# Performance work log

Hardware: AMD Instinct MI355X
Metric: run time of the kernel (lower is better)

Reference implementation:

```python
import jax, jax.numpy as jnp
import numpy as np
import math

B, H, T, D = 4, 16, 577, 1024   # CLIP ViT-L/336: 576 patches + CLS
NEED = 192                      # need_token_num
GROUP = NEED // 4               # 48 PCA components


def setup_inputs():
    key = jax.random.key(0)
    k1, k2 = jax.random.split(key)
    hidden_states = jax.random.normal(k1, (B, T, D), dtype=jnp.float32)
    attn = jax.random.uniform(k2, (B, H, T, T), dtype=jnp.float32)
    attn_weights = attn / attn.sum(-1, keepdims=True)  # row-stochastic attention
    return {"hidden_states": hidden_states, "attn_weights": attn_weights}


def batch_pca(hidden, q):
    # torch.pca_lowrank(sigmoid(h).transpose(2,1)[:,:,1:], q): center columns, top-q right singular vectors
    M = jax.nn.sigmoid(hidden.astype(jnp.float32)).transpose(0, 2, 1)[:, :, 1:]  # [B, D, N]
    Mc = M - M.mean(axis=1, keepdims=True)
    _, _, Vh = jnp.linalg.svd(Mc, full_matrices=False)      # [B, min(D,N), N]
    V = jnp.abs(jnp.transpose(Vh[:, :q, :], (0, 2, 1)))     # [B, N, q]
    belong = jnp.argmax(V, axis=-1)                          # [B, N]
    return V, belong


def batch_similarity_nms(group_sim, scores, threshold):
    # group_sim [B,G,N,N], scores [B,N,G], threshold [B]
    Bn, G, N, _ = group_sim.shape
    bi = jnp.arange(Bn)[:, None]
    gi = jnp.arange(G)[None, :]

    def cond(state):
        return state[0].sum() > 0

    def body(state):
        ns, rs, counts, gs = state
        max_values = ns.max(axis=1)          # [B,G]
        max_idx = jnp.argmax(ns, axis=1)     # [B,G]
        valid = max_values > 0
        sim_row = group_sim[bi, gi, max_idx]  # [B,G,N] row of selected token
        idx_n = jnp.where(valid, max_idx, N)  # sentinel -> dropped
        rs = rs.at[bi, idx_n, gi].set(gs, mode='drop')
        ns = ns.at[bi, idx_n, gi].set(0.0, mode='drop')
        suppress = sim_row > threshold[:, None, None]          # [B,G,N]
        ns = jnp.where(jnp.transpose(suppress, (0, 2, 1)), 0.0, ns)
        return ns, rs, counts + valid.astype(jnp.int32), gs - 1.0

    init = (scores, scores, jnp.zeros((Bn, G), jnp.int32), jnp.float32(1000.0))
    _, rs, counts, _ = jax.lax.while_loop(cond, body, init)
    return counts, rs  # kept-per-group counts, return_scores


def _forward(hs, attn):
    Bn, T_, _ = hs.shape
    N = T_ - 1
    need, G = NEED, GROUP
    hsc = jax.lax.stop_gradient(hs)
    attnc = jax.lax.stop_gradient(attn)

    V, belong = batch_pca(hsc, G)
    cls_sum = attnc[:, :, 0, 1:].sum(axis=1)                  # [B,N] cls attention
    onehot = belong[:, :, None] == jnp.arange(G)[None, None, :]  # [B,N,G]
    scores = jnp.where(onehot, cls_sum[:, :, None], 0.0).astype(jnp.float32)

    x = hsc[:, 1:, :]
    normalized = x / jnp.maximum(jnp.linalg.norm(x, axis=-1, keepdims=True), 1e-12)
    similarity = jnp.einsum('bnd,bmd->bnm', normalized, normalized).astype(jnp.float32)
    triu = jnp.triu(jnp.ones((N, N), bool), k=1)
    sim_mean = (similarity * triu).sum((-1, -2)) / triu.sum()  # [B]

    m = belong[:, None, :] == jnp.arange(G)[None, :, None]     # [B,G,N]
    mask4 = m[:, :, :, None] | m[:, :, None, :]                # row-or-col in group
    group_sim = jnp.where(mask4, similarity[:, None, :, :], 0.0)  # [B,G,N,N]

    keep_counts, ret_scores = batch_similarity_nms(group_sim, scores, (need / 32.0) * sim_mean)

    group_counts = onehot.sum(axis=1).astype(jnp.int32)        # [B,G]
    lower = jnp.minimum(1, group_counts)
    upper = jnp.minimum(jnp.minimum(5 * math.ceil(need / 64), group_counts), keep_counts)

    def ub_cond(u):
        return jnp.any(u.sum(-1) < need)

    def ub_body(u):
        deficient = (u.sum(-1) < need).astype(u.dtype)
        return jnp.minimum(u + deficient[:, None], group_counts)

    upper = jax.lax.while_loop(ub_cond, ub_body, upper)

    other = jnp.maximum(need - lower.sum(-1) - 1, 0)           # [B]
    norm_counts = keep_counts.astype(jnp.float32) / keep_counts.sum(-1, keepdims=True).astype(jnp.float32)
    csum = jnp.cumsum(norm_counts, axis=-1)
    od = jnp.round(csum * other[:, None].astype(jnp.float32)).astype(jnp.int32)
    od = od - jnp.concatenate([jnp.zeros((Bn, 1), jnp.int32), od[:, :-1]], axis=-1)
    token_d0 = jnp.minimum(od + lower, upper)
    sort_idx_g = jnp.argsort(-keep_counts, axis=-1)            # groups by kept count, desc
    target = other + lower.sum(-1)                             # == need-1 per batch
    bi1 = jnp.arange(Bn)

    def f_cond(state):
        return jnp.any(state[0].sum(-1) < target)

    def f_body(state):
        d, fg = state
        deficient = d.sum(-1) < target
        gidx = jnp.take_along_axis(sort_idx_g, jnp.minimum(fg, G - 1)[:, None], axis=1)[:, 0]
        fill = jnp.minimum(upper[bi1, gidx] - d[bi1, gidx], target - d.sum(-1))
        d = d.at[bi1, gidx].add(jnp.where(deficient, fill, 0))
        return d, fg + deficient.astype(fg.dtype)

    token_d, _ = jax.lax.while_loop(f_cond, f_body, (token_d0, jnp.zeros((Bn,), jnp.int32)))

    # top token_d[b,g] indices per group by return_scores, concatenated in group order
    sort_idx = jnp.transpose(jnp.argsort(-ret_scores, axis=1), (0, 2, 1)).astype(jnp.int32)  # [B,G,N]
    take = jnp.arange(N)[None, None, :] < token_d[:, :, None]  # [B,G,N]
    flat_take = take.reshape(Bn, G * N)
    flat_idx = sort_idx.reshape(Bn, G * N)
    L = need - 1  # token_d sums exactly to target == need-1
    pos = jnp.cumsum(flat_take, axis=1) - 1
    pos = jnp.where(flat_take, pos, L)
    gathered = jnp.zeros((Bn, L), jnp.int32).at[bi1[:, None], pos].set(flat_idx, mode='drop')
    batch_indices = jnp.concatenate([jnp.zeros((Bn, 1), jnp.int32), gathered + 1], axis=1)  # [B, need]
    out = jnp.take_along_axis(hs, batch_indices[:, :, None], axis=1)  # [B, need, D]
    return out, batch_indices


def reference(hidden_states, attn_weights):
    return _forward(hidden_states, attn_weights)
```

## Files before the change

kernel.cpp:

```cpp
#include <hip/hip_runtime.h>
#include <math.h>

constexpr int B_ = 4, T_ = 577, N_ = 576, D_ = 1024, G_ = 48, H_ = 16;
constexpr int NEED_ = 192, L_ = 191;
constexpr int TRIU_CNT = N_ * (N_ - 1) / 2;
constexpr int NB_ = 8;
constexpr int NBAR_ = 640;

constexpr size_t OF_MSIG = 0;
constexpr size_t OF_SIM  = OF_MSIG + (size_t)B_*N_*D_*4;
constexpr size_t OF_A    = OF_SIM  + (size_t)B_*N_*N_*4;
constexpr size_t OF_MS   = OF_A    + (size_t)B_*N_*N_*8;
constexpr size_t OF_INVN = OF_MS   + (size_t)B_*N_*8;
constexpr size_t OF_CLS  = OF_INVN + (size_t)B_*N_*8;
constexpr size_t OF_DT   = OF_CLS  + (size_t)B_*N_*4;
constexpr size_t OF_ET   = OF_DT   + (size_t)B_*N_*8;
constexpr size_t OF_TAU  = OF_ET   + (size_t)B_*N_*8;
constexpr size_t OF_EVAL = OF_TAU  + (size_t)B_*N_*8;
constexpr size_t OF_Z    = OF_EVAL + (size_t)B_*G_*8;
constexpr size_t OF_PART = OF_Z    + (size_t)B_*G_*N_*8;
constexpr size_t OF_THR  = OF_PART + (size_t)B_*36*8;
constexpr size_t OF_BEL  = OF_THR  + 64;
constexpr size_t OF_BAR  = OF_BEL  + (size_t)B_*N_*4;
constexpr size_t OF_FLG  = OF_BAR  + (size_t)B_*NBAR_*4;
constexpr size_t OF_VB   = OF_FLG  + (size_t)B_*16*4;
constexpr size_t OF_WB   = OF_VB   + (size_t)B_*N_*8;
constexpr size_t OF_SG   = OF_WB   + (size_t)B_*2*N_*8;
constexpr size_t OF_KP   = OF_SG   + (size_t)B_*8*8;
constexpr size_t WS_NEEDED = OF_KP + (size_t)B_*2*16*8;

constexpr size_t OF_PV_ALIAS = OF_MSIG + ((size_t)8 << 20);

__device__ __forceinline__ double blockReduceD(double x, double* red) {
  int lane = threadIdx.x & 63, wv = threadIdx.x >> 6;
  int nw = (blockDim.x + 63) >> 6;
  for (int o = 32; o > 0; o >>= 1) x += __shfl_down(x, o);
  __syncthreads();
  if (lane == 0) red[wv] = x;
  __syncthreads();
  double t = red[0];
  for (int i = 1; i < nw; i++) t += red[i];
  return t;
}

__device__ __forceinline__ void blockReduce4(double& x0, double& x1, double& x2,
                                             double& x3, double* red) {
  int lane = threadIdx.x & 63, wv = threadIdx.x >> 6;
  int nw = (blockDim.x + 63) >> 6;
  for (int o = 32; o > 0; o >>= 1) {
    x0 += __shfl_down(x0, o); x1 += __shfl_down(x1, o);
    x2 += __shfl_down(x2, o); x3 += __shfl_down(x3, o);
  }
  __syncthreads();
  if (lane == 0) { red[wv*4+0]=x0; red[wv*4+1]=x1; red[wv*4+2]=x2; red[wv*4+3]=x3; }
  __syncthreads();
  double t0 = red[0], t1 = red[1], t2 = red[2], t3 = red[3];
  for (int i = 1; i < nw; i++) {
    t0 += red[i*4+0]; t1 += red[i*4+1]; t2 += red[i*4+2]; t3 += red[i*4+3];
  }
  x0 = t0; x1 = t1; x2 = t2; x3 = t3;
}

__device__ __forceinline__ double cload(const double* p) {
  return __hip_atomic_load(p, __ATOMIC_RELAXED, __HIP_MEMORY_SCOPE_AGENT);
}
__device__ __forceinline__ void cstore(double* p, double x) {
  __hip_atomic_store(p, x, __ATOMIC_RELAXED, __HIP_MEMORY_SCOPE_AGENT);
}

__device__ __forceinline__ void gbar(int* bar, int slot, int tid) {
  __syncthreads();
  if (tid == 0) {
    __hip_atomic_fetch_add(&bar[slot], 1, __ATOMIC_RELAXED, __HIP_MEMORY_SCOPE_AGENT);
    while (__hip_atomic_load(&bar[slot], __ATOMIC_ACQUIRE, __HIP_MEMORY_SCOPE_AGENT) < NB_)
      __builtin_amdgcn_s_sleep(2);
  }
  __syncthreads();
  __asm__ volatile("" ::: "memory");
}

__global__ void k_prep(const float* __restrict__ hs, float* __restrict__ msig,
                       double* __restrict__ ms, double* __restrict__ invn,
                       int* __restrict__ bars) {
  __shared__ double red[16];
  if (blockIdx.x == 0) {
    for (int i = threadIdx.x; i < B_ * NBAR_; i += blockDim.x) bars[i] = 0;
  }
  int bn = blockIdx.x; int b = bn / N_, n = bn % N_;
  const float* row = hs + ((size_t)b*T_ + (n+1)) * (size_t)D_;
  float* mrow = msig + (size_t)bn * D_;
  double ssig = 0.0, ssq = 0.0;
  for (int d = threadIdx.x; d < D_; d += blockDim.x) {
    float x = row[d];
    float sg = 1.0f / (1.0f + expf(-x));
    mrow[d] = sg;
    ssig += (double)sg;
    ssq  += (double)x * (double)x;
  }
  double tot_sig = blockReduceD(ssig, red);
  double tot_sq  = blockReduceD(ssq, red);
  if (threadIdx.x == 0) {
    ms[bn] = tot_sig;
    invn[bn] = 1.0 / fmax(sqrt(tot_sq), 1e-12);
  }
}

__global__ void k_cls(const float* __restrict__ attn, float* __restrict__ cls) {
  int idx = blockIdx.x * blockDim.x + threadIdx.x;
  if (idx >= B_ * N_) return;
  int b = idx / N_, n = idx % N_;
  float s = 0.0f;
  for (int h = 0; h < H_; h++)
    s += attn[(((size_t)b*H_ + h) * T_ + 0) * T_ + (1 + n)];
  cls[idx] = s;
}

__global__ void k_gemm(const float* __restrict__ hs, const float* __restrict__ msig,
                       const double* __restrict__ ms, const double* __restrict__ invn,
                       double* __restrict__ Aout, float* __restrict__ sim, int mode) {
  __shared__ float As[32][17], Bs[32][17];
  int b = blockIdx.z;
  int bi0 = blockIdx.y * 32, bj0 = blockIdx.x * 32;
  const float* base = (mode == 0) ? (msig + (size_t)b*N_*D_)
                                  : (hs + ((size_t)b*T_ + 1) * (size_t)D_);
  int tid = threadIdx.x;
  int tx = tid & 15, ty = tid >> 4;
  double a00 = 0, a01 = 0, a10 = 0, a11 = 0;
  for (int k0 = 0; k0 < D_; k0 += 16) {
    int r = tid >> 4, c = tid & 15;
    As[r][c] = base[(size_t)(bi0 + r) * D_ + k0 + c];
    Bs[r][c] = base[(size_t)(bj0 + r) * D_ + k0 + c];
    int e = tid + 256; r = e >> 4; c = e & 15;
    As[r][c] = base[(size_t)(bi0 + r) * D_ + k0 + c];
    Bs[r][c] = base[(size_t)(bj0 + r) * D_ + k0 + c];
    __syncthreads();
#pragma unroll
    for (int kk = 0; kk < 16; kk++) {
      double x0 = As[2*ty][kk],   x1 = As[2*ty+1][kk];
      double y0 = Bs[2*tx][kk],   y1 = Bs[2*tx+1][kk];
      a00 += x0*y0; a01 += x0*y1; a10 += x1*y0; a11 += x1*y1;
    }
    __syncthreads();
  }
  int i0 = bi0 + 2*ty, j0 = bj0 + 2*tx;
  if (mode == 0) {
    const double* msb = ms + (size_t)b*N_;
    double* Ab = Aout + (size_t)b*N_*N_;
    const double inv1024 = 1.0 / 1024.0;
    Ab[(size_t)i0*N_ + j0]         = a00 - msb[i0]*msb[j0]*inv1024;
    Ab[(size_t)i0*N_ + j0+1]       = a01 - msb[i0]*msb[j0+1]*inv1024;
    Ab[(size_t)(i0+1)*N_ + j0]     = a10 - msb[i0+1]*msb[j0]*inv1024;
    Ab[(size_t)(i0+1)*N_ + j0+1]   = a11 - msb[i0+1]*msb[j0+1]*inv1024;
  } else {
    const double* iv = invn + (size_t)b*N_;
    float* sb = sim + (size_t)b*N_*N_;
    sb[(size_t)i0*N_ + j0]       = (float)(a00 * iv[i0]*iv[j0]);
    sb[(size_t)i0*N_ + j0+1]     = (float)(a01 * iv[i0]*iv[j0+1]);
    sb[(size_t)(i0+1)*N_ + j0]   = (float)(a10 * iv[i0+1]*iv[j0]);
    sb[(size_t)(i0+1)*N_ + j0+1] = (float)(a11 * iv[i0+1]*iv[j0+1]);
  }
}

__global__ void k_simsum(const float* __restrict__ sim, double* __restrict__ part) {
  __shared__ double red[4];
  int blk = blockIdx.x; int b = blk / 36, s = blk % 36;
  const float* sb = sim + (size_t)b*N_*N_;
  double p = 0.0;
  for (int i = s*16; i < s*16 + 16; i++) {
    const float* row = sb + (size_t)i*N_;
    for (int j = i + 1 + threadIdx.x; j < N_; j += blockDim.x) p += (double)row[j];
  }
  double t = blockReduceD(p, red);
  if (threadIdx.x == 0) part[blk] = t;
}

__global__ void k_thr(const double* __restrict__ part, float* __restrict__ thrF) {
  int b = threadIdx.x;
  if (b < B_) {
    double s = 0.0;
    for (int i = 0; i < 36; i++) s += part[b*36 + i];
    thrF[b] = 6.0f * (float)(s / (double)TRIU_CNT);
  }
}

__global__ __launch_bounds__(512) void k_tridiag_mb(double* __restrict__ Aall,
    double* __restrict__ dT, double* __restrict__ eT, double* __restrict__ tauT,
    double* __restrict__ pv_all, double* __restrict__ wb_all,
    int* __restrict__ bars) {
  __shared__ __attribute__((aligned(16))) double rb[3][N_];
  __shared__ __attribute__((aligned(16))) double wwb[2][N_];
  __shared__ double red[32];
  __shared__ double nx0s;
  int blk = blockIdx.x;
  int b = blk % B_;
  int t = blk / B_;
  double* A  = Aall + (size_t)b*N_*N_;
  double* dv = dT   + (size_t)b*N_;
  double* ev = eT   + (size_t)b*N_;
  double* tv = tauT + (size_t)b*N_;
  double* pvB = pv_all + (size_t)b*2*N_;
  double* wbB = wb_all + (size_t)b*2*N_;
  int* bar = bars + b*NBAR_;
  int tid = threadIdx.x, lane = tid & 63, wv = tid >> 6;

  double sig;
  {
    double ps = 0.0;
    if (tid == 0) nx0s = A[1];
    for (int j = tid; j < N_; j += 512) {
      rb[0][j] = 0.0;
      wwb[1][j] = 0.0;
      double a0 = A[j];
      rb[1][j] = a0;
      rb[2][j] = A[(size_t)N_ + j];
      if (j >= 1) ps += a0 * a0;
    }
    sig = blockReduceD(ps, red);
  }

  for (int k = 0; k < N_ - 2; k++) {
    int rot = k % 3;
    double* vp = rb[rot];
    double* vc = rb[(rot + 1) % 3];
    double* r2 = rb[(rot + 2) % 3];
    double* wp = wwb[(k & 1) ^ 1];
    double* wc = wwb[k & 1];
    double* wbk = wbB + (size_t)(k & 1) * N_;
    double* pvk = pvB + (size_t)(k & 1) * N_;

    double sigma = sig;
    double x0 = nx0s;
    double alpha, tauk;
    if (sigma == 0.0) { alpha = 0.0; tauk = 0.0; }
    else {
      alpha = (x0 >= 0.0) ? -sqrt(sigma) : sqrt(sigma);
      tauk = 1.0 / (sigma - alpha * x0);
    }
    if (tid == 0) {
      vc[k + 1] = x0 - alpha;
      if (t == 0) { dv[k] = vc[k]; ev[k] = alpha; tv[k] = tauk; }
    }
    __syncthreads();

    int rr = (k + 1) % NB_;
    int rofs = t - rr; if (rofs < 0) rofs += NB_;
    for (int r = (k + 1) + rofs + wv * NB_; r < N_; r += 8 * NB_) {
      double* Ar = A + (size_t)r * N_;
      double vrp = vp[r], wrp = wp[r];
      double pd = 0.0;
      int jbeg = k + 1;
      if (jbeg & 1) {
        if (lane == 0) {
          double nv = Ar[jbeg] - vrp * wp[jbeg] - wrp * vp[jbeg];
          Ar[jbeg] = nv;
          pd += nv * vc[jbeg];
        }
        jbeg++;
      }
      if (r == k + 2) {
        for (int j = jbeg + 2 * lane; j < N_; j += 128) {
          double2 av  = *(const double2*)(Ar + j);
          double2 wpv = *(const double2*)(wp + j);
          double2 vpv = *(const double2*)(vp + j);
          double2 vcv = *(const double2*)(vc + j);
          double nv0 = av.x - vrp * wpv.x - wrp * vpv.x;
          double nv1 = av.y - vrp * wpv.y - wrp * vpv.y;
          double2 st; st.x = nv0; st.y = nv1;
          *(double2*)(Ar + j) = st;
          pd += nv0 * vcv.x + nv1 * vcv.y;
          if (j > k + 1) cstore(&pvk[j], nv0);
          cstore(&pvk[j + 1], nv1);
        }
      } else {
        for (int j = jbeg + 2 * lane; j < N_; j += 128) {
          double2 av  = *(const double2*)(Ar + j);
          double2 wpv = *(const double2*)(wp + j);
          double2 vpv = *(const double2*)(vp + j);
          double2 vcv = *(const double2*)(vc + j);
          double nv0 = av.x - vrp * wpv.x - wrp * vpv.x;
          double nv1 = av.y - vrp * wpv.y - wrp * vpv.y;
          double2 st; st.x = nv0; st.y = nv1;
          *(double2*)(Ar + j) = st;
          pd += nv0 * vcv.x + nv1 * vcv.y;
        }
      }
      for (int o = 32; o > 0; o >>= 1) pd += __shfl_down(pd, o);
      if (lane == 0) cstore(&wbk[r], tauk * pd);
    }
    gbar(bar, k, tid);

    int i0 = k + 1 + tid;
    bool s0 = (i0 < N_), s1 = (i0 + 512 < N_);
    double w0 = s0 ? cload(&wbk[i0]) : 0.0;
    double w1 = s1 ? cload(&wbk[i0 + 512]) : 0.0;
    double p0 = (s0 && tid > 0) ? cload(&pvk[i0]) : 0.0;
    double p1 = s1 ? cload(&pvk[i0 + 512]) : 0.0;
    double wr1 = cload(&wbk[k + 1]);
    double wr2 = cload(&wbk[k + 2]);
    if ((k % NB_) == t)
      for (int j = k + 1 + tid; j < N_; j += 512) A[(size_t)k * N_ + j] = vc[j];
    double vc0 = s0 ? vc[i0] : 0.0;
    double vc1 = s1 ? vc[i0 + 512] : 0.0;
    double vk1 = vc[k + 1], vk2 = vc[k + 2];
    double r20 = s0 ? r2[i0] : 0.0;
    double r21 = s1 ? r2[i0 + 512] : 0.0;
    double a0v = r20 - vk1 * w0 - wr1 * vc0;
    double a1v = r21 - vk1 * w1 - wr1 * vc1;
    double kd = w0 * vc0 + w1 * vc1;
    double sa2 = 0.0, sav = 0.0, sv2 = 0.0;
    if (s0 && tid > 0) { sa2 += a0v*a0v; sav += a0v*vc0; sv2 += vc0*vc0; }
    if (s1)            { sa2 += a1v*a1v; sav += a1v*vc1; sv2 += vc1*vc1; }
    blockReduce4(kd, sa2, sav, sv2, red);
    double K = 0.5 * tauk * kd;
    double c = 2.0 * K * vk1;
    sig = sa2 + 2.0 * c * sav + c * c * sv2;
    double wk2 = wr2 - K * vk2;
    if (s0) {
      double wcj = w0 - K * vc0;
      wc[i0] = wcj;
      double nr1v = a0v + c * vc0;
      r2[i0] = nr1v;
      if (tid == 1) nx0s = nr1v;
      if (tid > 0) vp[i0] = p0 - vk2 * wcj - wk2 * vc0;
    }
    if (s1) {
      double wcj = w1 - K * vc1;
      wc[i0 + 512] = wcj;
      r2[i0 + 512] = a1v + c * vc1;
      vp[i0 + 512] = p1 - vk2 * wcj - wk2 * vc1;
    }
    __syncthreads();
  }

  if (t == 0 && tid == 0) {
    double* r1f = rb[((N_ - 3) + 2) % 3];
    double* r2f = rb[(N_ - 3) % 3];
    dv[N_-2] = r1f[N_-2];
    ev[N_-2] = r1f[N_-1];
    dv[N_-1] = r2f[N_-1];
    ev[N_-1] = 0.0; tv[N_-2] = 0.0; tv[N_-1] = 0.0;
  }
}

__global__ __launch_bounds__(64) void k_eigvals_ms(const double* __restrict__ dT,
    const double* __restrict__ eT, double* __restrict__ eval) {
  __shared__ double sd[N_], se2[N_];
  int blk = blockIdx.x; int b = blk / G_, j = blk % G_;
  int lane = threadIdx.x;
  for (int i = lane; i < N_; i += 64) {
    sd[i] = dT[(size_t)b*N_ + i];
    se2[i] = eT[(size_t)b*N_ + i];
  }
  __syncthreads();
  double lo = 1e300, hi = -1e300;
  for (int i = lane; i < N_; i += 64) {
    double r = ((i > 0) ? fabs(se2[i-1]) : 0.0) + ((i < N_-1) ? fabs(se2[i]) : 0.0);
    lo = fmin(lo, sd[i] - r); hi = fmax(hi, sd[i] + r);
  }
  for (int o = 32; o > 0; o >>= 1) {
    lo = fmin(lo, __shfl_xor(lo, o));
    hi = fmax(hi, __shfl_xor(hi, o));
  }
  double span = hi - lo + 1e-30;
  lo -= span * 1e-6; hi += span * 1e-6;
  __syncthreads();
  for (int i = lane; i < N_; i += 64) { double e = se2[i]; se2[i] = e * e; }
  __syncthreads();
  int target = N_ - 1 - j;
  for (int round = 0; round < 9; round++) {
    double width = hi - lo;
    double mid = lo + width * ((double)(lane + 1) / 65.0);
    double pm1 = 1.0;
    double pcur = sd[0] - mid;
    int cnt = (pcur <= 0.0) ? 1 : 0;
    if (pcur == 0.0) pcur = -1e-300;
    for (int i = 1; i < N_; i++) {
      double pnew = (sd[i] - mid) * pcur - se2[i-1] * pm1;
      bool chg = ((pnew < 0.0) != (pcur < 0.0)) || (pnew == 0.0);
      cnt += chg ? 1 : 0;
      if (pnew == 0.0) pnew = (pcur < 0.0) ? 1e-300 : -1e-300;
      pm1 = pcur; pcur = pnew;
      if ((i & 3) == 3) {
        double ap = fmax(fabs(pcur), fabs(pm1));
        double s = (ap > 1e160) ? 1e-160 : ((ap < 1e-160) ? 1e160 : 1.0);
        if (s != 1.0) {
          pcur *= s; pm1 *= s;
          if (pcur == 0.0) pcur = (pm1 < 0.0) ? 1e-300 : -1e-300;
          if (pm1 == 0.0)  pm1  = (pcur < 0.0) ? 1e-300 : -1e-300;
        }
      }
    }
    unsigned long long mask = __ballot(cnt > target);
    double nlo, nhi;
    if (mask == 0ULL) { nlo = lo + width * (64.0 / 65.0); nhi = hi; }
    else {
      int m = __ffsll(mask) - 1;
      nhi = lo + width * ((double)(m + 1) / 65.0);
      nlo = (m == 0) ? lo : lo + width * ((double)m / 65.0);
    }
    lo = nlo; hi = nhi;
  }
  if (lane == 0) eval[(size_t)b*G_ + j] = 0.5 * (lo + hi);
}

__global__ void k_eigvecs(const double* __restrict__ dT, const double* __restrict__ eT,
    const double* __restrict__ eval,
    double* __restrict__ Ud, double* __restrict__ U1, double* __restrict__ U2,
    double* __restrict__ Um, int* __restrict__ Ufl, double* __restrict__ Yv,
    double* __restrict__ Z) {
  __shared__ double sd[N_], se[N_];
  __shared__ double red0;
  __shared__ int cstart[G_];
  __shared__ double sh_ev[G_];
  int b = blockIdx.x;
  for (int i = threadIdx.x; i < N_; i += blockDim.x) {
    sd[i] = dT[(size_t)b*N_ + i]; se[i] = eT[(size_t)b*N_ + i];
  }
  if (threadIdx.x < G_) sh_ev[threadIdx.x] = eval[(size_t)b*G_ + threadIdx.x];
  __syncthreads();
  int j = threadIdx.x;
  size_t sbase = (size_t)b * N_ * G_;
  double* ud = Ud + sbase; double* u1 = U1 + sbase; double* u2 = U2 + sbase;
  double* um = Um + sbase; int* ufl = Ufl + sbase; double* yv = Yv + sbase;
  if (j < G_) {
    double lam = sh_ev[j];
    double GU = 1e-30 * (1.0 + fabs(lam));
    double ak = sd[0] - lam;
    double bk = se[0];
    for (int k = 0; k < N_ - 1; k++) {
      double sub = se[k];
      double diag1 = sd[k+1] - lam;
      double sup1 = (k < N_ - 2) ? se[k+1] : 0.0;
      double udv, u1v, u2v, umv; int flv;
      if (fabs(ak) >= fabs(sub)) {
        double piv = ak;
        if (fabs(piv) < GU) piv = (piv >= 0.0) ? GU : -GU;
        double rp = 1.0 / piv;
        double ml = sub * rp;
        udv = rp; u1v = bk; u2v = 0.0; umv = ml; flv = 0;
        ak = diag1 - ml * bk; bk = sup1;
      } else {
        double rs = 1.0 / sub;
        double ml = ak * rs;
        udv = rs; u1v = diag1; u2v = sup1; umv = ml; flv = 1;
        ak = bk - ml * diag1; bk = -ml * sup1;
      }
      ud[(size_t)k*G_+j] = udv; u1[(size_t)k*G_+j] = u1v; u2[(size_t)k*G_+j] = u2v;
      um[(size_t)k*G_+j] = umv; ufl[(size_t)k*G_+j] = flv;
    }
    { double piv = ak; if (fabs(piv) < GU) piv = (piv >= 0.0) ? GU : -GU;
      ud[(size_t)(N_-1)*G_+j] = 1.0 / piv; u1[(size_t)(N_-1)*G_+j] = 0.0; u2[(size_t)(N_-1)*G_+j] = 0.0; }
    for (int i = 0; i < N_; i++) {
      unsigned s = (unsigned)(i * 2654435761u) ^ (unsigned)((j + 1) * 40503u) ^ (unsigned)(b * 2246822519u);
      s = s * 1664525u + 1013904223u;
      s ^= s >> 16; s = s * 2246822519u;
      double rv = ((double)(s >> 8) * (1.0 / 16777216.0)) * 2.0 - 1.0;
      if (fabs(rv) < 1e-3) rv = 0.5;
      yv[(size_t)i*G_+j] = rv;
    }
    for (int it = 0; it < 3; it++) {
      if (it) {
        double mx = 0.0;
        for (int i = 0; i < N_; i++) mx = fmax(mx, fabs(yv[(size_t)i*G_+j]));
        double sc = 1.0 / fmax(mx, 1e-300);
        for (int i = 0; i < N_; i++) yv[(size_t)i*G_+j] *= sc;
      }
      double ykc = yv[0*G_ + j];
      for (int k = 0; k < N_ - 1; k++) {
        double ynx = yv[(size_t)(k+1)*G_+j];
        double yk = ykc, yk1 = ynx;
        if (ufl[(size_t)k*G_+j]) { yk = ynx; yk1 = ykc; }
        yk1 -= um[(size_t)k*G_+j] * yk;
        yv[(size_t)k*G_+j] = yk;
        ykc = yk1;
      }
      double y1, y2 = 0.0;
      { double tt = ykc * ud[(size_t)(N_-1)*G_+j];
        yv[(size_t)(N_-1)*G_+j] = tt; y1 = tt; }
      for (int k = N_ - 2; k >= 0; k--) {
        double tt = yv[(size_t)k*G_+j] - u1[(size_t)k*G_+j]*y1 - u2[(size_t)k*G_+j]*y2;
        tt *= ud[(size_t)k*G_+j];
        yv[(size_t)k*G_+j] = tt;
        y2 = y1; y1 = tt;
      }
    }
    double s2 = 0.0;
    for (int i = 0; i < N_; i++) { double tt = yv[(size_t)i*G_+j]; s2 += tt * tt; }
    double inv = 1.0 / sqrt(fmax(s2, 1e-300));
    double* Zj = Z + ((size_t)b*G_ + j) * N_;
    for (int i = 0; i < N_; i++) Zj[i] = yv[(size_t)i*G_+j] * inv;
  }
  __syncthreads();
  if (threadIdx.x == 0) {
    double tol = 1e-10 * (fabs(sh_ev[0]) + 1.0);
    cstart[0] = 0;
    for (int q = 1; q < G_; q++)
      cstart[q] = ((sh_ev[q-1] - sh_ev[q]) < tol) ? cstart[q-1] : q;
  }
  __syncthreads();
  for (int q = 1; q < G_; q++) {
    if (cstart[q] == q) continue;
    double* Zq = Z + ((size_t)b*G_ + q) * N_;
    for (int p = cstart[q]; p < q; p++) {
      double* Zp = Z + ((size_t)b*G_ + p) * N_;
      double dp = 0.0;
      for (int i = threadIdx.x; i < N_; i += blockDim.x) dp += Zq[i] * Zp[i];
      for (int o = 32; o > 0; o >>= 1) dp += __shfl_down(dp, o);
      if (threadIdx.x == 0) red0 = dp;
      __syncthreads();
      double dd = red0;
      for (int i = threadIdx.x; i < N_; i += blockDim.x) Zq[i] -= dd * Zp[i];
      __syncthreads();
    }
    double s2 = 0.0;
    for (int i = threadIdx.x; i < N_; i += blockDim.x) { double tt = Zq[i]; s2 += tt * tt; }
    for (int o = 32; o > 0; o >>= 1) s2 += __shfl_down(s2, o);
    if (threadIdx.x == 0) red0 = s2;
    __syncthreads();
    double inv = 1.0 / sqrt(fmax(red0, 1e-300));
    for (int i = threadIdx.x; i < N_; i += blockDim.x) Zq[i] *= inv;
    __syncthreads();
  }
}

__global__ __launch_bounds__(64) void k_backxf_mb(const double* __restrict__ Aall,
    const double* __restrict__ tauT, double* __restrict__ Z) {
  int blk = blockIdx.x;
  int b = blk / G_, q = blk % G_;
  const double* A = Aall + (size_t)b*N_*N_;
  const double* tau = tauT + (size_t)b*N_;
  double* Zq = Z + ((size_t)b*G_ + q) * N_;
  int lane = threadIdx.x;
  double z[9];
#pragma unroll
  for (int m = 0; m < 9; m++) z[m] = Zq[lane + 64*m];
  for (int k = N_ - 3; k >= 0; k--) {
    double t = tau[k];
    if (t == 0.0) continue;
    const double* vk = A + (size_t)k*N_;
    double vv[9]; double p = 0.0;
#pragma unroll
    for (int m = 0; m < 9; m++) {
      int i = lane + 64*m;
      double vi = (i > k) ? vk[i] : 0.0;
      vv[m] = vi; p += vi * z[m];
    }
    for (int o = 32; o > 0; o >>= 1) p += __shfl_down(p, o);
    p = __shfl(p, 0);
    double s = t * p;
#pragma unroll
    for (int m = 0; m < 9; m++) z[m] -= s * vv[m];
  }
#pragma unroll
  for (int m = 0; m < 9; m++) Zq[lane + 64*m] = z[m];
}

__global__ void k_belong(const double* __restrict__ Z, int* __restrict__ belong) {
  int idx = blockIdx.x * blockDim.x + threadIdx.x;
  if (idx >= B_ * N_) return;
  int b = idx / N_, n = idx % N_;
  const double* Zb = Z + (size_t)b*G_*N_;
  double best = -1.0; int bi = 0;
  for (int q = 0; q < G_; q++) {
    double av = fabs(Zb[(size_t)q*N_ + n]);
    if (av > best) { best = av; bi = q; }
  }
  belong[idx] = bi;
}

__global__ __launch_bounds__(256) void k_nms(const float* __restrict__ sim,
    const float* __restrict__ cls, const int* __restrict__ belong,
    const float* __restrict__ thrF, float* __restrict__ outF) {
  __shared__ float nsv[N_], rsv[N_];
  __shared__ int bl_s[N_];
  __shared__ int lists[N_];
  __shared__ int off[G_ + 1];
  __shared__ int kc[G_], gc[G_], lowv[G_], upv[G_], tokd[G_], sortg[G_], pre[G_ + 1];
  __shared__ int gathered[L_];
  __shared__ int anyv;
  __shared__ float shthr;
  int b = blockIdx.x, tid = threadIdx.x;
  const float* simb = sim + (size_t)b*N_*N_;
  if (tid == 0) shthr = thrF[b];
  if (tid < G_) gc[tid] = 0;
  __syncthreads();
  for (int i = tid; i < N_; i += 256) {
    int g = belong[b*N_ + i];
    bl_s[i] = g;
    float sc = cls[b*N_ + i];
    nsv[i] = sc; rsv[i] = sc;
    atomicAdd(&gc[g], 1);
  }
  __syncthreads();
  if (tid == 0) {
    off[0] = 0;
    for (int g = 0; g < G_; g++) off[g+1] = off[g] + gc[g];
    for (int g = 0; g < G_; g++) pre[g] = off[g];
    for (int n = 0; n < N_; n++) lists[pre[bl_s[n]]++] = n;
  }
  __syncthreads();
  float thr = shthr;
  float gs = 1000.0f;
  int myc = 0;
  for (int iter = 0; iter < N_ + 8; iter++) {
    if (tid == 0) anyv = 0;
    __syncthreads();
    int m = -1;
    if (tid < G_) {
      float mx = 0.0f;
      for (int a = off[tid]; a < off[tid+1]; a++) {
        int n2 = lists[a];
        float vv = nsv[n2];
        if (vv > mx) { mx = vv; m = n2; }
      }
      if (m >= 0) anyv = 1;
    }
    __syncthreads();
    if (m >= 0) {
      rsv[m] = gs;
      nsv[m] = 0.0f;
      const float* srow = simb + (size_t)m*N_;
      for (int a = off[tid]; a < off[tid+1]; a++) {
        int n2 = lists[a];
        if (nsv[n2] > 0.0f && srow[n2] > thr) nsv[n2] = 0.0f;
      }
      myc++;
    }
    gs -= 1.0f;
    __syncthreads();
    if (!anyv) break;
  }
  if (tid < G_) kc[tid] = myc;
  __syncthreads();
  if (tid == 0) {
    int sumkc = 0; for (int g = 0; g < G_; g++) sumkc += kc[g];
    int sumlow = 0;
    for (int g = 0; g < G_; g++) {
      lowv[g] = (gc[g] < 1) ? gc[g] : 1;
      int u = 15; if (gc[g] < u) u = gc[g]; if (kc[g] < u) u = kc[g];
      upv[g] = u; sumlow += lowv[g];
    }
    int su = 0; for (int g = 0; g < G_; g++) su += upv[g];
    while (su < NEED_) {
      su = 0;
      for (int g = 0; g < G_; g++) { int u = upv[g] + 1; if (u > gc[g]) u = gc[g]; upv[g] = u; su += u; }
    }
    int other = NEED_ - sumlow - 1; if (other < 0) other = 0;
    float s = (float)sumkc;
    float c = 0.0f; int prevR = 0;
    float otherf = (float)other;
    for (int g = 0; g < G_; g++) {
      float nc = (float)kc[g] / s;
      c += nc;
      int R = (int)rintf(c * otherf);
      int od = R - prevR; prevR = R;
      int t0 = od + lowv[g]; if (t0 > upv[g]) t0 = upv[g];
      tokd[g] = t0;
    }
    for (int g = 0; g < G_; g++) sortg[g] = g;
    for (int a = 1; a < G_; a++) {
      int vIdx = sortg[a]; int key = kc[vIdx]; int p2 = a - 1;
      while (p2 >= 0 && kc[sortg[p2]] < key) { sortg[p2+1] = sortg[p2]; p2--; }
      sortg[p2+1] = vIdx;
    }
    int target = other + sumlow;
    int sumd = 0; for (int g = 0; g < G_; g++) sumd += tokd[g];
    int fg = 0;
    while (sumd < target) {
      int gi = sortg[(fg < G_-1) ? fg : (G_-1)];
      int fill = upv[gi] - tokd[gi];
      int rem = target - sumd;
      if (rem < fill) fill = rem;
      tokd[gi] += fill; sumd += fill;
      fg++;
      if (fg > 100000) break;
    }
    pre[0] = 0; for (int g = 0; g < G_; g++) pre[g+1] = pre[g] + tokd[g];
  }
  __syncthreads();
  for (int i = tid; i < L_; i += 256) gathered[i] = 0;
  __syncthreads();
  if (tid < G_) {
    int g = tid;
    int td = tokd[g], base = pre[g];
    for (int t = 0; t < td; t++) {
      float bv = -3e38f; int bn2 = 0;
      for (int a = off[g]; a < off[g+1]; a++) {
        int n2 = lists[a];
        float vv = rsv[n2];
        if (vv > bv) { bv = vv; bn2 = n2; }
      }
      rsv[bn2] = -3e38f;
      int pos = base + t;
      if (pos < L_) gathered[pos] = bn2;
    }
  }
  __syncthreads();
  if (tid < NEED_) {
    float val = (tid == 0) ? 0.0f : (float)(gathered[tid - 1] + 1);
    outF[(size_t)B_*NEED_*D_ + (size_t)b*NEED_ + tid] = val;
  }
}

__global__ void k_gather(const float* __restrict__ hs, float* __restrict__ outF) {
  int blk = blockIdx.x;
  int b = blk / NEED_, i = blk % NEED_;
  int idx = (int)outF[(size_t)B_*NEED_*D_ + (size_t)b*NEED_ + i];
  const float4* src = (const float4*)(hs + ((size_t)b*T_ + idx) * (size_t)D_);
  float4* dst = (float4*)(outF + ((size_t)b*NEED_ + i) * (size_t)D_);
  dst[threadIdx.x] = src[threadIdx.x];
}

extern "C" void kernel_launch(void* const* d_in, const int* in_sizes, int n_in,
                              void* d_out, int out_size, void* d_ws, size_t ws_size,
                              hipStream_t stream) {
  if (ws_size < WS_NEEDED) return;
  const float* hs   = (const float*)d_in[0];
  const float* attn = (const float*)d_in[1];
  float* outF = (float*)d_out;
  char* w = (char*)d_ws;
  float*  msig = (float*)(w + OF_MSIG);
  float*  sim  = (float*)(w + OF_SIM);
  double* A    = (double*)(w + OF_A);
  double* ms   = (double*)(w + OF_MS);
  double* invn = (double*)(w + OF_INVN);
  float*  cls  = (float*)(w + OF_CLS);
  double* dT   = (double*)(w + OF_DT);
  double* eT   = (double*)(w + OF_ET);
  double* tauT = (double*)(w + OF_TAU);
  double* eval = (double*)(w + OF_EVAL);
  double* Z    = (double*)(w + OF_Z);
  double* part = (double*)(w + OF_PART);
  float*  thrF = (float*)(w + OF_THR);
  int*    belong = (int*)(w + OF_BEL);
  int*    bars = (int*)(w + OF_BAR);
  double* wb   = (double*)(w + OF_WB);
  double* pv   = (double*)(w + OF_PV_ALIAS);
  double* Ud = (double*)(w + OF_MSIG);
  double* U1 = Ud + (size_t)B_*N_*G_;
  double* U2 = U1 + (size_t)B_*N_*G_;
  double* Um = U2 + (size_t)B_*N_*G_;
  double* Yv = Um + (size_t)B_*N_*G_;
  int*    Ufl = (int*)(Yv + (size_t)B_*N_*G_);

  k_prep<<<B_*N_, 256, 0, stream>>>(hs, msig, ms, invn, bars);
  k_cls<<<(B_*N_ + 255)/256, 256, 0, stream>>>(attn, cls);
  k_gemm<<<dim3(N_/32, N_/32, B_), 256, 0, stream>>>(hs, msig, ms, invn, A, sim, 0);
  k_gemm<<<dim3(N_/32, N_/32, B_), 256, 0, stream>>>(hs, msig, ms, invn, A, sim, 1);
  k_simsum<<<B_*36, 256, 0, stream>>>(sim, part);
  k_thr<<<1, 64, 0, stream>>>(part, thrF);
  k_tridiag_mb<<<B_*NB_, 512, 0, stream>>>(A, dT, eT, tauT, pv, wb, bars);
  k_eigvals_ms<<<B_*G_, 64, 0, stream>>>(dT, eT, eval);
  k_eigvecs<<<B_, 64, 0, stream>>>(dT, eT, eval, Ud, U1, U2, Um, Ufl, Yv, Z);
  k_backxf_mb<<<B_*G_, 64, 0, stream>>>(A, tauT, Z);
  k_belong<<<(B_*N_ + 255)/256, 256, 0, stream>>>(Z, belong);
  k_nms<<<B_, 256, 0, stream>>>(sim, cls, belong, thrF, outF);
  k_gather<<<B_*NEED_, 256, 0, stream>>>(hs, outF);
}
```

Measured before the change: 7.352 ms.

## Co-schedule similarity GEMM and CLS sum as extra blocks inside tridiagonalization kernel

The cosine-similarity GEMM (mode 1) and the CLS attention sum now run as extra blocks appended to the tridiagonalization launch, with their shared memory overlaid through a union. The aim is to use idle CUs while the 32 latency-bound tridiagonalization blocks run, and to drop two separate launches. The trade-off is that the tridiag blocks, which rely on inter-block barriers, must still all be resident and run alongside the GEMM blocks. Those GEMM blocks also use only half of their 512 threads for compute.

```diff
diff --git a/kernel.cpp b/kernel.cpp
--- a/kernel.cpp
+++ b/kernel.cpp
@@ -6,6 +6,12 @@
 constexpr int TRIU_CNT = N_ * (N_ - 1) / 2;
 constexpr int NB_ = 8;
 constexpr int NBAR_ = 640;
+
+constexpr int TRI_BLKS = B_ * NB_;
+constexpr int GM_BX = N_ / 32;
+constexpr int GM_BLKS = GM_BX * GM_BX * B_;
+constexpr int CLS_BLKS = (B_ * N_ + 511) / 512;
+constexpr int FUSED_BLKS = TRI_BLKS + GM_BLKS + CLS_BLKS;
 
 constexpr size_t OF_MSIG = 0;
 constexpr size_t OF_SIM  = OF_MSIG + (size_t)B_*N_*D_*4;
@@ -103,16 +109,6 @@
     ms[bn] = tot_sig;
     invn[bn] = 1.0 / fmax(sqrt(tot_sq), 1e-12);
   }
-}
-
-__global__ void k_cls(const float* __restrict__ attn, float* __restrict__ cls) {
-  int idx = blockIdx.x * blockDim.x + threadIdx.x;
-  if (idx >= B_ * N_) return;
-  int b = idx / N_, n = idx % N_;
-  float s = 0.0f;
-  for (int h = 0; h < H_; h++)
-    s += attn[(((size_t)b*H_ + h) * T_ + 0) * T_ + (1 + n)];
-  cls[idx] = s;
 }
 
 __global__ void k_gemm(const float* __restrict__ hs, const float* __restrict__ msig,
@@ -183,14 +179,81 @@
   }
 }
 
+union __align__(16) SharedU {
+  struct {
+    double rb[3][N_];
+    double wwb[2][N_];
+    double red[32];
+    double nx0s;
+  } tri;
+  struct {
+    float As[32][17];
+    float Bs[32][17];
+  } gm;
+};
+
 __global__ __launch_bounds__(512) void k_tridiag_mb(double* __restrict__ Aall,
     double* __restrict__ dT, double* __restrict__ eT, double* __restrict__ tauT,
     double* __restrict__ pv_all, double* __restrict__ wb_all,
-    int* __restrict__ bars) {
-  __shared__ __attribute__((aligned(16))) double rb[3][N_];
-  __shared__ __attribute__((aligned(16))) double wwb[2][N_];
-  __shared__ double red[32];
-  __shared__ double nx0s;
+    int* __restrict__ bars,
+    const float* __restrict__ hs, const double* __restrict__ invn,
+    float* __restrict__ sim, const float* __restrict__ attn,
+    float* __restrict__ cls) {
+  __shared__ SharedU sh;
+  int tid = threadIdx.x;
+
+  if (blockIdx.x >= TRI_BLKS && blockIdx.x < TRI_BLKS + GM_BLKS) {
+    int gblk = blockIdx.x - TRI_BLKS;
+    int bx = gblk % GM_BX, by = (gblk / GM_BX) % GM_BX, b = gblk / (GM_BX * GM_BX);
+    int bi0 = by * 32, bj0 = bx * 32;
+    const float* base = hs + ((size_t)b*T_ + 1) * (size_t)D_;
+    float (&As)[32][17] = sh.gm.As;
+    float (&Bs)[32][17] = sh.gm.Bs;
+    int tx = tid & 15, ty = (tid < 256) ? (tid >> 4) : 0;
+    double a00 = 0, a01 = 0, a10 = 0, a11 = 0;
+    int r = tid >> 5;
+    for (int k0 = 0; k0 < D_; k0 += 16) {
+      int lr = tid >> 4, lc = tid & 15;
+      As[lr][lc] = base[(size_t)(bi0 + lr) * D_ + k0 + lc];
+      Bs[lr][lc] = base[(size_t)(bj0 + lr) * D_ + k0 + lc];
+      __syncthreads();
+      if (tid < 256) {
+#pragma unroll
+        for (int kk = 0; kk < 16; kk++) {
+          double x0 = As[2*ty][kk],   x1 = As[2*ty+1][kk];
+          double y0 = Bs[2*tx][kk],   y1 = Bs[2*tx+1][kk];
+          a00 += x0*y0; a01 += x0*y1; a10 += x1*y0; a11 += x1*y1;
+        }
+      }
+      __syncthreads();
+    }
+    if (tid < 256) {
+      int i0 = bi0 + 2*ty, j0 = bj0 + 2*tx;
+      const double* iv = invn + (size_t)b*N_;
+      float* sb = sim + (size_t)b*N_*N_;
+      sb[(size_t)i0*N_ + j0]       = (float)(a00 * iv[i0]*iv[j0]);
+      sb[(size_t)i0*N_ + j0+1]     = (float)(a01 * iv[i0]*iv[j0+1]);
+      sb[(size_t)(i0+1)*N_ + j0]   = (float)(a10 * iv[i0+1]*iv[j0]);
+      sb[(size_t)(i0+1)*N_ + j0+1] = (float)(a11 * iv[i0+1]*iv[j0+1]);
+    }
+    return;
+  }
+
+  if (blockIdx.x >= TRI_BLKS + GM_BLKS) {
+    int idx = (blockIdx.x - (TRI_BLKS + GM_BLKS)) * 512 + tid;
+    if (idx < B_ * N_) {
+      int b = idx / N_, n = idx % N_;
+      float s = 0.0f;
+      for (int h = 0; h < H_; h++)
+        s += attn[(((size_t)b*H_ + h) * T_ + 0) * T_ + (1 + n)];
+      cls[idx] = s;
+    }
+    return;
+  }
+
+  double (&rb)[3][N_] = sh.tri.rb;
+  double (&wwb)[2][N_] = sh.tri.wwb;
+  double* red = sh.tri.red;
   int blk = blockIdx.x;
   int b = blk % B_;
   int t = blk / B_;
@@ -201,12 +264,12 @@
   double* pvB = pv_all + (size_t)b*2*N_;
   double* wbB = wb_all + (size_t)b*2*N_;
   int* bar = bars + b*NBAR_;
-  int tid = threadIdx.x, lane = tid & 63, wv = tid >> 6;
+  int lane = tid & 63, wv = tid >> 6;
 
   double sig;
   {
     double ps = 0.0;
-    if (tid == 0) nx0s = A[1];
+    if (tid == 0) sh.tri.nx0s = A[1];
     for (int j = tid; j < N_; j += 512) {
       rb[0][j] = 0.0;
       wwb[1][j] = 0.0;
@@ -229,7 +292,7 @@
     double* pvk = pvB + (size_t)(k & 1) * N_;
 
     double sigma = sig;
-    double x0 = nx0s;
+    double x0 = sh.tri.nx0s;
     double alpha, tauk;
     if (sigma == 0.0) { alpha = 0.0; tauk = 0.0; }
     else {
@@ -320,7 +383,7 @@
       wc[i0] = wcj;
       double nr1v = a0v + c * vc0;
       r2[i0] = nr1v;
-      if (tid == 1) nx0s = nr1v;
+      if (tid == 1) sh.tri.nx0s = nr1v;
       if (tid > 0) vp[i0] = p0 - vk2 * wcj - wk2 * vc0;
     }
     if (s1) {
@@ -744,12 +807,11 @@
   int*    Ufl = (int*)(Yv + (size_t)B_*N_*G_);
 
   k_prep<<<B_*N_, 256, 0, stream>>>(hs, msig, ms, invn, bars);
-  k_cls<<<(B_*N_ + 255)/256, 256, 0, stream>>>(attn, cls);
   k_gemm<<<dim3(N_/32, N_/32, B_), 256, 0, stream>>>(hs, msig, ms, invn, A, sim, 0);
-  k_gemm<<<dim3(N_/32, N_/32, B_), 256, 0, stream>>>(hs, msig, ms, invn, A, sim, 1);
+  k_tridiag_mb<<<FUSED_BLKS, 512, 0, stream>>>(A, dT, eT, tauT, pv, wb, bars,
+                                               hs, invn, sim, attn, cls);
   k_simsum<<<B_*36, 256, 0, stream>>>(sim, part);
   k_thr<<<1, 64, 0, stream>>>(part, thrF);
-  k_tridiag_mb<<<B_*NB_, 512, 0, stream>>>(A, dT, eT, tauT, pv, wb, bars);
   k_eigvals_ms<<<B_*G_, 64, 0, stream>>>(dT, eT, eval);
   k_eigvecs<<<B_, 64, 0, stream>>>(dT, eT, eval, Ud, U1, U2, Um, Ufl, Yv, Z);
   k_backxf_mb<<<B_*G_, 64, 0, stream>>>(A, tauT, Z);
```

After: 7.225 ms. Within noise of the previous version (-1.7%).
